# Kernel optimization log

Measured on AMD Instinct MI355X. Metric: run time of the kernel, lower is better.

## Reference

```python
import jax, jax.numpy as jnp
import numpy as np

B, S, D, H = 4, 2048, 1024, 16
HD = D // H
DFF = 4 * D
EPS = 1e-5


def setup_inputs() -> dict:
    key = jax.random.key(0)
    ks = jax.random.split(key, 8)
    s = 0.02
    return {
        "x": jax.random.normal(ks[0], (B, S, D), dtype=jnp.float32),
        "ln1_g": jnp.ones((D,), jnp.float32),
        "ln1_b": jnp.zeros((D,), jnp.float32),
        "Wq": jax.random.normal(ks[1], (D, D), jnp.float32) * s,
        "Wk": jax.random.normal(ks[2], (D, D), jnp.float32) * s,
        "Wv": jax.random.normal(ks[3], (D, D), jnp.float32) * s,
        "Wo": jax.random.normal(ks[4], (D, D), jnp.float32) * s,
        "ln2_g": jnp.ones((D,), jnp.float32),
        "ln2_b": jnp.zeros((D,), jnp.float32),
        "W1": jax.random.normal(ks[5], (D, DFF), jnp.float32) * s,
        "b1": jnp.zeros((DFF,), jnp.float32),
        "W2": jax.random.normal(ks[6], (DFF, D), jnp.float32) * s,
        "b2": jnp.zeros((D,), jnp.float32),
    }


def _layernorm(x, g, b):
    mu = jnp.mean(x, axis=-1, keepdims=True)
    var = jnp.var(x, axis=-1, keepdims=True)
    return (x - mu) * jax.lax.rsqrt(var + EPS) * g + b


def _block(x, ln1_g, ln1_b, Wq, Wk, Wv, Wo, ln2_g, ln2_b, W1, b1, W2, b2):
    # --- attention sub-block (pre-norm) ---
    h = _layernorm(x, ln1_g, ln1_b)
    q = (h @ Wq).reshape(B, S, H, HD)
    k = (h @ Wk).reshape(B, S, H, HD)
    v = (h @ Wv).reshape(B, S, H, HD)
    scores = jnp.einsum("bqhd,bkhd->bhqk", q, k) / np.sqrt(HD).astype(np.float32)
    causal = jnp.tril(jnp.ones((S, S), dtype=bool))
    scores = jnp.where(causal, scores, -jnp.inf)
    attn = jax.nn.softmax(scores, axis=-1)  # dropout p=0 (eval)
    ctx = jnp.einsum("bhqk,bkhd->bqhd", attn, v).reshape(B, S, D)
    x = x + ctx @ Wo
    # --- FFN sub-block (pre-norm) ---
    h = _layernorm(x, ln2_g, ln2_b)
    h = jax.nn.gelu(h @ W1 + b1, approximate=False)  # torch nn.GELU() = exact erf
    return x + (h @ W2 + b2)


def reference(x, ln1_g, ln1_b, Wq, Wk, Wv, Wo, ln2_g, ln2_b, W1, b1, W2, b2):
    return _block(x, ln1_g, ln1_b, Wq, Wk, Wv, Wo, ln2_g, ln2_b, W1, b1, W2, b2)
```

## Files before the change

kernel.cpp:

```cpp
#include <hip/hip_runtime.h>
#include <hip/hip_bf16.h>
#include <math.h>

#define NB 4
#define NS 2048
#define ND 1024
#define NH 16
#define NHD 64
#define NDFF 4096
#define QKS 3072

typedef __attribute__((ext_vector_type(8))) short bf16x8;
typedef __attribute__((ext_vector_type(4))) float f32x4;
typedef __attribute__((ext_vector_type(16))) float f32x16;
typedef __attribute__((ext_vector_type(4))) short short4v;
typedef __attribute__((ext_vector_type(4))) int i32x4;

#define QSCL 0.18033688011112042f

static __device__ __forceinline__ short f2b(float f) {
  union { __hip_bfloat16 b; short s; } u;
  u.b = __float2bfloat16(f);
  return u.s;
}
static __device__ __forceinline__ float b2f(short s) {
  union { float f; unsigned u; } v;
  v.u = ((unsigned)(unsigned short)s) << 16;
  return v.f;
}

static __device__ __forceinline__ int cvtpk(float lo, float hi_) {
  int r;
  asm("v_cvt_pk_bf16_f32 %0, %1, %2" : "=v"(r) : "v"(lo), "v"(hi_));
  return r;
}

static __device__ __forceinline__ float pairsum(float x) {
  auto r = __builtin_amdgcn_permlane32_swap(__float_as_uint(x), __float_as_uint(x), false, false);
  return __uint_as_float(r[0]) + __uint_as_float(r[1]);
}

static __device__ __forceinline__ float gelu_t(float v) {
  const float u = v * (0.7978845608f + 0.0356774081f * v * v);
  return v / (1.0f + __expf(-2.0f * u));
}

template <bool BF16IN>
__global__ __launch_bounds__(256) void ln_kernel(
    const void* __restrict__ xin, const float* __restrict__ g,
    const float* __restrict__ b, short* __restrict__ out) {
  __shared__ float red[8];
  const int row = blockIdx.x;
  const int t = threadIdx.x;
  float xv[4];
  if (BF16IN) {
    const short4v sv = *(const short4v*)((const short*)xin + (size_t)row * ND + t * 4);
#pragma unroll
    for (int i = 0; i < 4; ++i) xv[i] = b2f(sv[i]);
  } else {
    const float4 fv = *(const float4*)((const float*)xin + (size_t)row * ND + t * 4);
    xv[0] = fv.x; xv[1] = fv.y; xv[2] = fv.z; xv[3] = fv.w;
  }
  float s = xv[0] + xv[1] + xv[2] + xv[3];
  float ss = xv[0] * xv[0] + xv[1] * xv[1] + xv[2] * xv[2] + xv[3] * xv[3];
#pragma unroll
  for (int m = 32; m >= 1; m >>= 1) {
    s += __shfl_xor(s, m);
    ss += __shfl_xor(ss, m);
  }
  if ((t & 63) == 0) { red[(t >> 6) * 2] = s; red[(t >> 6) * 2 + 1] = ss; }
  __syncthreads();
  s = red[0] + red[2] + red[4] + red[6];
  ss = red[1] + red[3] + red[5] + red[7];
  const float mu = s * (1.0f / ND);
  const float var = ss * (1.0f / ND) - mu * mu;
  const float rs = rsqrtf(var + 1e-5f);
  const float4 gv = *(const float4*)(g + t * 4);
  const float4 bv = *(const float4*)(b + t * 4);
  short o[4];
  o[0] = f2b((xv[0] - mu) * rs * gv.x + bv.x);
  o[1] = f2b((xv[1] - mu) * rs * gv.y + bv.y);
  o[2] = f2b((xv[2] - mu) * rs * gv.z + bv.z);
  o[3] = f2b((xv[3] - mu) * rs * gv.w + bv.w);
  *(short4v*)(out + (size_t)row * ND + t * 4) = *(short4v*)o;
}

__global__ __launch_bounds__(256) void tcast_kernel(
    const float* __restrict__ in, short* __restrict__ out, int K, int N) {
  __shared__ float tile[32][33];
  const int n0 = blockIdx.x * 32, k0 = blockIdx.y * 32;
  const int tx = threadIdx.x & 31, ty = threadIdx.x >> 5;
#pragma unroll
  for (int i = 0; i < 32; i += 8)
    tile[ty + i][tx] = in[(size_t)(k0 + ty + i) * N + n0 + tx];
  __syncthreads();
#pragma unroll
  for (int i = 0; i < 32; i += 8)
    out[(size_t)(n0 + ty + i) * K + k0 + tx] = f2b(tile[tx][ty + i]);
}

__global__ __launch_bounds__(256) void tcast4_kernel(
    const float* __restrict__ w0, const float* __restrict__ w1,
    const float* __restrict__ w2, const float* __restrict__ w3,
    short* __restrict__ dqkv, short* __restrict__ dwo) {
  __shared__ float tile[32][33];
  const int z = blockIdx.z;
  const float* in = (z == 0) ? w0 : (z == 1) ? w1 : (z == 2) ? w2 : w3;
  short* out = (z < 3) ? dqkv + (size_t)z * 1024 * 1024 : dwo;
  const int n0 = blockIdx.x * 32, k0 = blockIdx.y * 32;
  const int tx = threadIdx.x & 31, ty = threadIdx.x >> 5;
#pragma unroll
  for (int i = 0; i < 32; i += 8)
    tile[ty + i][tx] = in[(size_t)(k0 + ty + i) * 1024 + n0 + tx];
  __syncthreads();
#pragma unroll
  for (int i = 0; i < 32; i += 8)
    out[(size_t)(n0 + ty + i) * 1024 + k0 + tx] = f2b(tile[tx][ty + i]);
}

__global__ __launch_bounds__(256) void vtrans_kernel(
    const short* __restrict__ in, short* __restrict__ out) {
  __shared__ short tile[64][72];
  const int s0 = blockIdx.x * 64, bh = blockIdx.y;
  const int bb = bh >> 4, hh = bh & 15;
  const int rr = threadIdx.x >> 3, cc = (threadIdx.x & 7) * 8;
#pragma unroll
  for (int it = 0; it < 2; ++it) {
    const int r = rr + it * 32;
    *(bf16x8*)&tile[r][cc] =
        *(const bf16x8*)&in[((size_t)(bb * NS + s0 + r)) * QKS + 2048 + hh * NHD + cc];
  }
  __syncthreads();
  const size_t ob = (size_t)bh * NHD * NS;
#pragma unroll
  for (int it = 0; it < 2; ++it) {
    const int d = rr + it * 32;
    short o[8];
#pragma unroll
    for (int j = 0; j < 8; ++j) o[j] = tile[cc + j][d];
    *(bf16x8*)&out[ob + (size_t)d * NS + s0 + cc] = *(bf16x8*)o;
  }
}

__device__ __forceinline__ void gload16(const void* g, void* l) {
  __builtin_amdgcn_global_load_lds(
      (const __attribute__((address_space(1))) unsigned int*)g,
      (__attribute__((address_space(3))) unsigned int*)l, 16, 0, 0);
}

template <int GM, int GN, int EPI, bool QS = false>
__global__ __launch_bounds__(256, 3) void gemms_kernel(
    const short* __restrict__ A, const short* __restrict__ Bt,
    float* __restrict__ Cf, short* __restrict__ Cb,
    const float* __restrict__ bias, const float* __restrict__ resf,
    const short* __restrict__ resb, int M, int N, int K) {
  __shared__ short lds[2 * 128 * 64];
  const int tid = threadIdx.x, l = tid & 63, w = tid >> 6;
  const int wm = w >> 1, wn = w & 1;
  const int nbm = M >> 7, nbn = N >> 7, nwg = nbm * nbn;
  int wg = blockIdx.x;
  wg = (wg & 7) * (nwg >> 3) + (wg >> 3);
  const int gidx = wg / (GM * GN), r = wg % (GM * GN);
  const int ngn = nbn / GN;
  const int bm = (gidx / ngn) * GM + r / GN;
  const int bn = (gidx % ngn) * GN + r % GN;

  const int srow = tid >> 3;
  const int sslot = (tid & 7) ^ (srow & 7);
  const short* Asrc = A + (size_t)(bm * 128 + srow) * K + sslot * 8;
  const short* Bsrc = Bt + (size_t)(bn * 128 + srow) * K + sslot * 8;
  const int wdst = w * 512;

  const int fr = l & 15, fg4 = l >> 4;
  int arow[4], brow[4];
#pragma unroll
  for (int i = 0; i < 4; ++i) {
    arow[i] = wm * 64 + i * 16 + fr;
    brow[i] = wn * 64 + i * 16 + fr;
  }

  f32x4 acc[4][4] = {};
  const int NT = K >> 6;

#pragma unroll
  for (int j = 0; j < 4; ++j) {
    gload16(Asrc, &lds[j * 2048 + wdst]);
    gload16(Bsrc, &lds[8192 + j * 2048 + wdst]);
    Asrc += (size_t)32 * K;
    Bsrc += (size_t)32 * K;
  }
  Asrc -= (size_t)128 * K;
  Bsrc -= (size_t)128 * K;

  for (int t = 0; t < NT; ++t) {
    __syncthreads();
#pragma unroll
    for (int kh = 0; kh < 2; ++kh) {
      bf16x8 af[4], bf[4];
#pragma unroll
      for (int i = 0; i < 4; ++i) {
        af[i] = *(const bf16x8*)&lds[arow[i] * 64 + (((kh * 4 + fg4) ^ (arow[i] & 7)) << 3)];
        bf[i] = *(const bf16x8*)&lds[8192 + brow[i] * 64 + (((kh * 4 + fg4) ^ (brow[i] & 7)) << 3)];
      }
      __builtin_amdgcn_s_setprio(1);
#pragma unroll
      for (int mi = 0; mi < 4; ++mi)
#pragma unroll
        for (int ni = 0; ni < 4; ++ni)
          acc[mi][ni] = __builtin_amdgcn_mfma_f32_16x16x32_bf16(bf[ni], af[mi], acc[mi][ni], 0, 0, 0);
      __builtin_amdgcn_s_setprio(0);
    }
    __syncthreads();
    if (t + 1 < NT) {
      const short* a = Asrc + (size_t)(t + 1) * 64;
      const short* b = Bsrc + (size_t)(t + 1) * 64;
#pragma unroll
      for (int j = 0; j < 4; ++j) {
        gload16(a, &lds[j * 2048 + wdst]);
        gload16(b, &lds[8192 + j * 2048 + wdst]);
        a += (size_t)32 * K;
        b += (size_t)32 * K;
      }
    }
  }

  const int fq = fg4 * 4;
  const int wrb = bm * 128 + wm * 64;
  const int wcb = bn * 128 + wn * 64;
#pragma unroll
  for (int mi = 0; mi < 4; ++mi) {
    const int row = wrb + mi * 16 + fr;
#pragma unroll
    for (int ni = 0; ni < 4; ++ni) {
      const int col = wcb + ni * 16 + fq;
      const f32x4 v = acc[mi][ni];
      if (EPI == 0) {
        const float scl = (QS && col < 1024) ? QSCL : 1.0f;
        short o[4];
#pragma unroll
        for (int rr = 0; rr < 4; ++rr) o[rr] = f2b(v[rr] * scl);
        *(short4v*)&Cb[(size_t)row * N + col] = *(short4v*)o;
      } else if (EPI == 1) {
        const f32x4 rv = *(const f32x4*)&resf[(size_t)row * N + col];
        short o[4];
#pragma unroll
        for (int rr = 0; rr < 4; ++rr) o[rr] = f2b(v[rr] + rv[rr]);
        *(short4v*)&Cb[(size_t)row * N + col] = *(short4v*)o;
      } else if (EPI == 2) {
        const f32x4 bv = *(const f32x4*)&bias[col];
        short o[4];
#pragma unroll
        for (int rr = 0; rr < 4; ++rr) o[rr] = f2b(gelu_t(v[rr] + bv[rr]));
        *(short4v*)&Cb[(size_t)row * N + col] = *(short4v*)o;
      } else {
        const f32x4 bv = *(const f32x4*)&bias[col];
        const short4v rv = *(const short4v*)&resb[(size_t)row * N + col];
        f32x4 o;
#pragma unroll
        for (int rr = 0; rr < 4; ++rr) o[rr] = v[rr] + bv[rr] + b2f(rv[rr]);
        *(f32x4*)&Cf[(size_t)row * N + col] = o;
      }
    }
  }
}

__global__ __launch_bounds__(256, 4) void attn_kernel(
    const short* __restrict__ qkv, const short* __restrict__ vt, short* __restrict__ ctx) {
  __shared__ short Kls[2][64 * 64];
  __shared__ short Vls[2][64 * 64];

  const int bid = blockIdx.x;
  const int bh = (bid & 7) * 8 + ((bid >> 3) & 7);
  const int ch = 15 - (bid >> 6);
  const int bb = bh >> 4, hh = bh & 15;
  const int lane = threadIdx.x & 63, wave = threadIdx.x >> 6;
  const int ql = lane & 31, hi = lane >> 5;
  const int qb0 = ch * 128 + wave * 32;

  bf16x8 qf[4];
  {
    const size_t qrow = ((size_t)bb * NS + qb0 + ql) * QKS + hh * NHD;
#pragma unroll
    for (int st = 0; st < 4; ++st)
      qf[st] = *(const bf16x8*)&qkv[qrow + st * 16 + hi * 8];
  }

  f32x16 acc[2] = {};
  float l_run = 0.f;

  const int srow = lane >> 3;
  const int sslot = (lane & 7) ^ srow;
  const short* kbasep = qkv + (size_t)bb * NS * QKS + 1024 + hh * NHD + sslot * 8;
  const short* vbasep = vt + (size_t)bh * NHD * NS + sslot * 8;

  const int nkt = (ch + 1) * 2;
#pragma unroll
  for (int r = 0; r < 2; ++r) {
    const int row = r * 32 + wave * 8 + srow;
    gload16(kbasep + (size_t)row * QKS, &Kls[0][(r * 32 + wave * 8) * 64]);
    gload16(vbasep + (size_t)row * NS, &Vls[0][(r * 32 + wave * 8) * 64]);
  }

  int buf = 0;
  for (int jt = 0; jt < nkt; ++jt) {
    asm volatile("s_waitcnt vmcnt(0) lgkmcnt(0)\n\ts_barrier" ::: "memory");
    if (jt + 1 < nkt) {
      const int k0n = (jt + 1) * 64;
#pragma unroll
      for (int r = 0; r < 2; ++r) {
        const int row = r * 32 + wave * 8 + srow;
        gload16(kbasep + (size_t)(k0n + row) * QKS, &Kls[buf ^ 1][(r * 32 + wave * 8) * 64]);
        gload16(vbasep + (size_t)row * NS + k0n, &Vls[buf ^ 1][(r * 32 + wave * 8) * 64]);
      }
    }
    const int k0 = jt * 64;
    const short* Kb = &Kls[buf][0];
    const short* Vb = &Vls[buf][0];
#pragma unroll
    for (int ks = 0; ks < 2; ++ks) {
      const int kbase = k0 + ks * 32;
      if (kbase > qb0) continue;
      bf16x8 kf[4], vf[2][2];
      const int krow = ks * 32 + ql;
#pragma unroll
      for (int st = 0; st < 4; ++st)
        kf[st] = *(const bf16x8*)&Kb[krow * 64 + ((st * 2 + hi) ^ (krow & 7)) * 8];
#pragma unroll
      for (int db = 0; db < 2; ++db) {
        const int vrow = db * 32 + ql;
#pragma unroll
        for (int su = 0; su < 2; ++su)
          vf[db][su] =
              *(const bf16x8*)&Vb[vrow * 64 + ((ks * 4 + su * 2 + hi) ^ (vrow & 7)) * 8];
      }
      const int qg = qb0 + ql;
      f32x16 s = {};
      __builtin_amdgcn_s_setprio(1);
#pragma unroll
      for (int st = 0; st < 4; ++st)
        s = __builtin_amdgcn_mfma_f32_32x32x16_bf16(kf[st], qf[st], s, 0, 0, 0);
      __builtin_amdgcn_s_setprio(0);
      const bool masked = (kbase + 31 > qb0);
      float pe[16];
      float lt = 0.f;
#pragma unroll
      for (int r = 0; r < 16; ++r) {
        float sv = s[r];
        if (masked) {
          const int key = kbase + 4 * hi + (r & 3) + 8 * (r >> 2);
          sv = (key > qg) ? -1e38f : sv;
        }
        pe[r] = exp2f(sv);
        lt += pe[r];
      }
      l_run += pairsum(lt);
      bf16x8 pf[2];
#pragma unroll
      for (int su = 0; su < 2; ++su) {
        const int a0 = cvtpk(pe[su * 8 + 0], pe[su * 8 + 1]);
        const int a1 = cvtpk(pe[su * 8 + 2], pe[su * 8 + 3]);
        const int b0 = cvtpk(pe[su * 8 + 4], pe[su * 8 + 5]);
        const int b1 = cvtpk(pe[su * 8 + 6], pe[su * 8 + 7]);
        auto r0 = __builtin_amdgcn_permlane32_swap((unsigned)a0, (unsigned)b0, false, false);
        auto r1 = __builtin_amdgcn_permlane32_swap((unsigned)a1, (unsigned)b1, false, false);
        union { i32x4 w; bf16x8 v; } u;
        u.w[0] = r0[0]; u.w[1] = r1[0]; u.w[2] = r0[1]; u.w[3] = r1[1];
        pf[su] = u.v;
      }
      __builtin_amdgcn_s_setprio(1);
#pragma unroll
      for (int su = 0; su < 2; ++su) {
        acc[0] = __builtin_amdgcn_mfma_f32_32x32x16_bf16(vf[0][su], pf[su], acc[0], 0, 0, 0);
        acc[1] = __builtin_amdgcn_mfma_f32_32x32x16_bf16(vf[1][su], pf[su], acc[1], 0, 0, 0);
      }
      __builtin_amdgcn_s_setprio(0);
    }
    buf ^= 1;
  }

  {
    const float inv = 1.0f / l_run;
    const size_t ob = ((size_t)bb * NS + qb0 + ql) * ND + hh * NHD + hi * 8;
#pragma unroll
    for (int db = 0; db < 2; ++db) {
#pragma unroll
      for (int J = 0; J < 2; ++J) {
        const int a0 = cvtpk(acc[db][J * 8 + 0] * inv, acc[db][J * 8 + 1] * inv);
        const int a1 = cvtpk(acc[db][J * 8 + 2] * inv, acc[db][J * 8 + 3] * inv);
        const int b0 = cvtpk(acc[db][J * 8 + 4] * inv, acc[db][J * 8 + 5] * inv);
        const int b1 = cvtpk(acc[db][J * 8 + 6] * inv, acc[db][J * 8 + 7] * inv);
        auto r0 = __builtin_amdgcn_permlane32_swap((unsigned)a0, (unsigned)b0, false, false);
        auto r1 = __builtin_amdgcn_permlane32_swap((unsigned)a1, (unsigned)b1, false, false);
        union { i32x4 w; bf16x8 v; } u;
        u.w[0] = r0[0]; u.w[1] = r1[0]; u.w[2] = r0[1]; u.w[3] = r1[1];
        *(bf16x8*)&ctx[ob + db * 32 + J * 16] = u.v;
      }
    }
  }
}

extern "C" void kernel_launch(void* const* d_in, const int* in_sizes, int n_in,
                              void* d_out, int out_size, void* d_ws, size_t ws_size,
                              hipStream_t stream) {
  (void)in_sizes; (void)n_in; (void)out_size; (void)ws_size;
  const float* x     = (const float*)d_in[0];
  const float* ln1_g = (const float*)d_in[1];
  const float* ln1_b = (const float*)d_in[2];
  const float* Wq    = (const float*)d_in[3];
  const float* Wk    = (const float*)d_in[4];
  const float* Wv    = (const float*)d_in[5];
  const float* Wo    = (const float*)d_in[6];
  const float* ln2_g = (const float*)d_in[7];
  const float* ln2_b = (const float*)d_in[8];
  const float* W1    = (const float*)d_in[9];
  const float* b1    = (const float*)d_in[10];
  const float* W2    = (const float*)d_in[11];
  const float* b2    = (const float*)d_in[12];
  float* out = (float*)d_out;

  char* ws = (char*)d_ws;
  const size_t MiB = 1024 * 1024;
  short* wqkvT = (short*)(ws + 0 * MiB);
  short* woT   = (short*)(ws + 6 * MiB);
  short* w1T   = (short*)(ws + 8 * MiB);
  short* w2T   = (short*)(ws + 16 * MiB);
  short* h     = (short*)(ws + 24 * MiB);
  short* ctx   = (short*)(ws + 24 * MiB);
  short* qkv   = (short*)(ws + 40 * MiB);
  short* vt    = (short*)(ws + 88 * MiB);
  short* hff   = (short*)(ws + 40 * MiB);
  short* x1b   = (short*)(ws + 104 * MiB);

  tcast4_kernel<<<dim3(32, 32, 4), 256, 0, stream>>>(Wq, Wk, Wv, Wo, wqkvT, woT);
  tcast_kernel<<<dim3(128, 32), 256, 0, stream>>>(W1, w1T, 1024, 4096);
  tcast_kernel<<<dim3(32, 128), 256, 0, stream>>>(W2, w2T, 4096, 1024);

  ln_kernel<false><<<8192, 256, 0, stream>>>(x, ln1_g, ln1_b, h);

  gemms_kernel<4, 6, 0, true><<<1536, 256, 0, stream>>>(h, wqkvT, nullptr, qkv, nullptr,
                                                        nullptr, nullptr, 8192, 3072, 1024);
  vtrans_kernel<<<dim3(32, 64), 256, 0, stream>>>(qkv, vt);

  attn_kernel<<<1024, 256, 0, stream>>>(qkv, vt, ctx);

  gemms_kernel<4, 8, 1><<<512, 256, 0, stream>>>(ctx, woT, nullptr, x1b, nullptr,
                                                 x, nullptr, 8192, 1024, 1024);

  ln_kernel<true><<<8192, 256, 0, stream>>>(x1b, ln2_g, ln2_b, h);

  gemms_kernel<4, 8, 2><<<2048, 256, 0, stream>>>(h, w1T, nullptr, hff, b1,
                                                  nullptr, nullptr, 8192, 4096, 1024);
  gemms_kernel<2, 2, 3><<<512, 256, 0, stream>>>(hff, w2T, out, nullptr, b2,
                                                 nullptr, x1b, 8192, 1024, 4096);
}
```

Measured before the change: 347.1 us.

## Double-buffer GEMM LDS with K=32 tiles and fuse V transpose into QKV epilogue

The GEMM main loop switches from a single 128x64 LDS tile with two barriers per step to a double-buffered 128x32 tile, so the next tile's global-to-LDS load is issued before the MFMAs on the current one and one barrier per step is removed. The LDS swizzle is rewritten for the 32-wide rows, and occupancy is raised to 4 waves-per-SIMD launch bounds. The separate V transpose kernel is removed: the QKV GEMM epilogue writes V columns directly into the transposed layout. Those scattered 2-byte stores are strided by the sequence length and poorly coalesced, and halving the K tile doubles the barrier count per K.

```diff
diff --git a/kernel.cpp b/kernel.cpp
--- a/kernel.cpp
+++ b/kernel.cpp
@@ -118,43 +118,20 @@
     out[(size_t)(n0 + ty + i) * 1024 + k0 + tx] = f2b(tile[tx][ty + i]);
 }
 
-__global__ __launch_bounds__(256) void vtrans_kernel(
-    const short* __restrict__ in, short* __restrict__ out) {
-  __shared__ short tile[64][72];
-  const int s0 = blockIdx.x * 64, bh = blockIdx.y;
-  const int bb = bh >> 4, hh = bh & 15;
-  const int rr = threadIdx.x >> 3, cc = (threadIdx.x & 7) * 8;
-#pragma unroll
-  for (int it = 0; it < 2; ++it) {
-    const int r = rr + it * 32;
-    *(bf16x8*)&tile[r][cc] =
-        *(const bf16x8*)&in[((size_t)(bb * NS + s0 + r)) * QKS + 2048 + hh * NHD + cc];
-  }
-  __syncthreads();
-  const size_t ob = (size_t)bh * NHD * NS;
-#pragma unroll
-  for (int it = 0; it < 2; ++it) {
-    const int d = rr + it * 32;
-    short o[8];
-#pragma unroll
-    for (int j = 0; j < 8; ++j) o[j] = tile[cc + j][d];
-    *(bf16x8*)&out[ob + (size_t)d * NS + s0 + cc] = *(bf16x8*)o;
-  }
-}
-
 __device__ __forceinline__ void gload16(const void* g, void* l) {
   __builtin_amdgcn_global_load_lds(
       (const __attribute__((address_space(1))) unsigned int*)g,
       (__attribute__((address_space(3))) unsigned int*)l, 16, 0, 0);
 }
 
-template <int GM, int GN, int EPI, bool QS = false>
-__global__ __launch_bounds__(256, 3) void gemms_kernel(
+template <int GM, int GN, int EPI>
+__global__ __launch_bounds__(256, 4) void gemmf_kernel(
     const short* __restrict__ A, const short* __restrict__ Bt,
     float* __restrict__ Cf, short* __restrict__ Cb,
     const float* __restrict__ bias, const float* __restrict__ resf,
-    const short* __restrict__ resb, int M, int N, int K) {
-  __shared__ short lds[2 * 128 * 64];
+    const short* __restrict__ resb, short* __restrict__ vtout,
+    int M, int N, int K) {
+  __shared__ short lds[2][8192];
   const int tid = threadIdx.x, l = tid & 63, w = tid >> 6;
   const int wm = w >> 1, wn = w & 1;
   const int nbm = M >> 7, nbn = N >> 7, nwg = nbm * nbn;
@@ -165,63 +142,52 @@
   const int bm = (gidx / ngn) * GM + r / GN;
   const int bn = (gidx % ngn) * GN + r % GN;
 
-  const int srow = tid >> 3;
-  const int sslot = (tid & 7) ^ (srow & 7);
+  const int srow = tid >> 2;
+  const int sslot = (tid & 3) ^ ((srow >> 1) & 3);
   const short* Asrc = A + (size_t)(bm * 128 + srow) * K + sslot * 8;
   const short* Bsrc = Bt + (size_t)(bn * 128 + srow) * K + sslot * 8;
   const int wdst = w * 512;
 
   const int fr = l & 15, fg4 = l >> 4;
-  int arow[4], brow[4];
+  int aoff[4], boff[4];
 #pragma unroll
   for (int i = 0; i < 4; ++i) {
-    arow[i] = wm * 64 + i * 16 + fr;
-    brow[i] = wn * 64 + i * 16 + fr;
-  }
+    const int ra = wm * 64 + i * 16 + fr;
+    const int rb = wn * 64 + i * 16 + fr;
+    aoff[i] = ra * 32 + ((fg4 ^ ((ra >> 1) & 3)) << 3);
+    boff[i] = 4096 + rb * 32 + ((fg4 ^ ((rb >> 1) & 3)) << 3);
+  }
+
+  auto stage = [&](int t, int bsel) {
+    short* d = &lds[bsel][0];
+    const short* a = Asrc + (size_t)t * 32;
+    const short* b = Bsrc + (size_t)t * 32;
+    gload16(a, d + wdst);
+    gload16(a + (size_t)64 * K, d + 2048 + wdst);
+    gload16(b, d + 4096 + wdst);
+    gload16(b + (size_t)64 * K, d + 6144 + wdst);
+  };
 
   f32x4 acc[4][4] = {};
-  const int NT = K >> 6;
-
-#pragma unroll
-  for (int j = 0; j < 4; ++j) {
-    gload16(Asrc, &lds[j * 2048 + wdst]);
-    gload16(Bsrc, &lds[8192 + j * 2048 + wdst]);
-    Asrc += (size_t)32 * K;
-    Bsrc += (size_t)32 * K;
-  }
-  Asrc -= (size_t)128 * K;
-  Bsrc -= (size_t)128 * K;
-
+  const int NT = K >> 5;
+  stage(0, 0);
   for (int t = 0; t < NT; ++t) {
     __syncthreads();
-#pragma unroll
-    for (int kh = 0; kh < 2; ++kh) {
-      bf16x8 af[4], bf[4];
-#pragma unroll
-      for (int i = 0; i < 4; ++i) {
-        af[i] = *(const bf16x8*)&lds[arow[i] * 64 + (((kh * 4 + fg4) ^ (arow[i] & 7)) << 3)];
-        bf[i] = *(const bf16x8*)&lds[8192 + brow[i] * 64 + (((kh * 4 + fg4) ^ (brow[i] & 7)) << 3)];
-      }
-      __builtin_amdgcn_s_setprio(1);
-#pragma unroll
-      for (int mi = 0; mi < 4; ++mi)
-#pragma unroll
-        for (int ni = 0; ni < 4; ++ni)
-          acc[mi][ni] = __builtin_amdgcn_mfma_f32_16x16x32_bf16(bf[ni], af[mi], acc[mi][ni], 0, 0, 0);
-      __builtin_amdgcn_s_setprio(0);
+    if (t + 1 < NT) stage(t + 1, (t + 1) & 1);
+    const short* cur = &lds[t & 1][0];
+    bf16x8 af[4], bf[4];
+#pragma unroll
+    for (int i = 0; i < 4; ++i) {
+      af[i] = *(const bf16x8*)(cur + aoff[i]);
+      bf[i] = *(const bf16x8*)(cur + boff[i]);
     }
-    __syncthreads();
-    if (t + 1 < NT) {
-      const short* a = Asrc + (size_t)(t + 1) * 64;
-      const short* b = Bsrc + (size_t)(t + 1) * 64;
-#pragma unroll
-      for (int j = 0; j < 4; ++j) {
-        gload16(a, &lds[j * 2048 + wdst]);
-        gload16(b, &lds[8192 + j * 2048 + wdst]);
-        a += (size_t)32 * K;
-        b += (size_t)32 * K;
-      }
-    }
+    __builtin_amdgcn_s_setprio(1);
+#pragma unroll
+    for (int mi = 0; mi < 4; ++mi)
+#pragma unroll
+      for (int ni = 0; ni < 4; ++ni)
+        acc[mi][ni] = __builtin_amdgcn_mfma_f32_16x16x32_bf16(bf[ni], af[mi], acc[mi][ni], 0, 0, 0);
+    __builtin_amdgcn_s_setprio(0);
   }
 
   const int fq = fg4 * 4;
@@ -235,10 +201,9 @@
       const int col = wcb + ni * 16 + fq;
       const f32x4 v = acc[mi][ni];
       if (EPI == 0) {
-        const float scl = (QS && col < 1024) ? QSCL : 1.0f;
         short o[4];
 #pragma unroll
-        for (int rr = 0; rr < 4; ++rr) o[rr] = f2b(v[rr] * scl);
+        for (int rr = 0; rr < 4; ++rr) o[rr] = f2b(v[rr]);
         *(short4v*)&Cb[(size_t)row * N + col] = *(short4v*)o;
       } else if (EPI == 1) {
         const f32x4 rv = *(const f32x4*)&resf[(size_t)row * N + col];
@@ -252,13 +217,27 @@
 #pragma unroll
         for (int rr = 0; rr < 4; ++rr) o[rr] = f2b(gelu_t(v[rr] + bv[rr]));
         *(short4v*)&Cb[(size_t)row * N + col] = *(short4v*)o;
-      } else {
+      } else if (EPI == 3) {
         const f32x4 bv = *(const f32x4*)&bias[col];
         const short4v rv = *(const short4v*)&resb[(size_t)row * N + col];
         f32x4 o;
 #pragma unroll
         for (int rr = 0; rr < 4; ++rr) o[rr] = v[rr] + bv[rr] + b2f(rv[rr]);
         *(f32x4*)&Cf[(size_t)row * N + col] = o;
+      } else {
+        if (wcb >= 2048) {
+          const int vcol = col - 2048;
+          const int vh = vcol >> 6, vd = vcol & 63;
+          short* vb = vtout + (((size_t)((row >> 11) * 16 + vh)) * 64 + vd) * NS + (row & 2047);
+#pragma unroll
+          for (int rr = 0; rr < 4; ++rr) vb[(size_t)rr * NS] = f2b(v[rr]);
+        } else {
+          const float scl = (col < 1024) ? QSCL : 1.0f;
+          short o[4];
+#pragma unroll
+          for (int rr = 0; rr < 4; ++rr) o[rr] = f2b(v[rr] * scl);
+          *(short4v*)&Cb[(size_t)row * N + col] = *(short4v*)o;
+        }
       }
     }
   }
@@ -437,19 +416,18 @@
 
   ln_kernel<false><<<8192, 256, 0, stream>>>(x, ln1_g, ln1_b, h);
 
-  gemms_kernel<4, 6, 0, true><<<1536, 256, 0, stream>>>(h, wqkvT, nullptr, qkv, nullptr,
-                                                        nullptr, nullptr, 8192, 3072, 1024);
-  vtrans_kernel<<<dim3(32, 64), 256, 0, stream>>>(qkv, vt);
+  gemmf_kernel<4, 6, 4><<<1536, 256, 0, stream>>>(h, wqkvT, nullptr, qkv, nullptr,
+                                                  nullptr, nullptr, vt, 8192, 3072, 1024);
 
   attn_kernel<<<1024, 256, 0, stream>>>(qkv, vt, ctx);
 
-  gemms_kernel<4, 8, 1><<<512, 256, 0, stream>>>(ctx, woT, nullptr, x1b, nullptr,
-                                                 x, nullptr, 8192, 1024, 1024);
+  gemmf_kernel<4, 8, 1><<<512, 256, 0, stream>>>(ctx, woT, nullptr, x1b, nullptr,
+                                                 x, nullptr, nullptr, 8192, 1024, 1024);
 
   ln_kernel<true><<<8192, 256, 0, stream>>>(x1b, ln2_g, ln2_b, h);
 
-  gemms_kernel<4, 8, 2><<<2048, 256, 0, stream>>>(h, w1T, nullptr, hff, b1,
-                                                  nullptr, nullptr, 8192, 4096, 1024);
-  gemms_kernel<2, 2, 3><<<512, 256, 0, stream>>>(hff, w2T, out, nullptr, b2,
-                                                 nullptr, x1b, 8192, 1024, 4096);
-}
+  gemmf_kernel<4, 8, 2><<<2048, 256, 0, stream>>>(h, w1T, nullptr, hff, b1,
+                                                  nullptr, nullptr, nullptr, 8192, 4096, 1024);
+  gemmf_kernel<2, 2, 3><<<512, 256, 0, stream>>>(hff, w2T, out, nullptr, b2,
+                                                 nullptr, x1b, nullptr, 8192, 1024, 4096);
+}
```

After: 352.7 us. Within noise of the previous version (+1.6%).
